# Kernel tuning notes

Hardware: AMD Instinct MI355X
Metric: run time of the kernel (lower is better)

Reference implementation:

```python
import jax, jax.numpy as jnp
import numpy as np

ROUTES = 1152
CAPS = 10
IN_CH = 8
OUT_CH = 16
BATCH = 256
NUM_ITER = 3


def setup_inputs() -> dict:
    key = jax.random.key(0)
    kx, kw = jax.random.split(key)
    x = jax.random.normal(kx, (BATCH, ROUTES, IN_CH), dtype=jnp.float32)
    # W corresponds to nn.Parameter of shape [1, routes, caps, out, in]; leading 1 dropped.
    W = jax.random.normal(kw, (ROUTES, CAPS, OUT_CH, IN_CH), dtype=jnp.float32)
    return {"x": x, "W": W}


def _squash(s):
    # Faithful to source: sum of squares over the trailing singleton dim -> elementwise.
    sq = s * s
    return sq * s / ((1.0 + sq) * jnp.sqrt(sq))


def reference(x, W):
    # u_hat[b,r,c,o] = W[r,c,o,i] @ x[b,r,i]
    u_hat = jnp.einsum("rcoi,bri->brco", W, x)
    b_ij = jnp.zeros((ROUTES, CAPS), dtype=x.dtype)
    v = None
    for it in range(NUM_ITER):
        # legacy F.softmax on 4D [1,R,C,1] tensor -> softmax over dim=1 (routes)
        c_ij = jax.nn.softmax(b_ij, axis=0)  # [R, C]
        s_j = jnp.einsum("rc,brco->bco", c_ij, u_hat)  # [B, C, O]
        v = _squash(s_j)
        if it < NUM_ITER - 1:
            # a_ij[b,r,c] = <u_hat[b,r,c,:], v[b,c,:]>; b_ij += mean over batch
            a_ij = jnp.einsum("brco,bco->brc", u_hat, v)
            b_ij = b_ij + a_ij.mean(axis=0)
    # original returns v_j.squeeze(1) with shape [B, caps, out, 1]
    return v[..., None]
```

## Files before the change

### kernel.cpp

```cpp
#include <hip/hip_runtime.h>
#include <math.h>

namespace {

constexpr int B_ = 256;
constexpr int R_ = 1152;
constexpr int C_ = 10;
constexpr int O_ = 16;
constexpr int I_ = 8;
constexpr int CO_ = C_ * O_;
constexpr int WRI_ = C_ * O_ * I_;

constexpr int KS2_ = 64;
constexpr int RC2_ = R_ / KS2_;
constexpr int RT_  = 4;
constexpr int NBLK_ = 640;

constexpr int KSF_ = 16;
constexpr int RCF_ = R_ / KSF_;
constexpr int MBF_ = 16;

constexpr size_t XT_OFF    = 0;
constexpr size_t XT_N      = (size_t)R_ * B_ * I_;
constexpr size_t SP_OFF    = XT_OFF + XT_N;
constexpr size_t SP_N      = (size_t)CO_ * KS2_ * B_;
constexpr size_t V_OFF     = SP_OFF + SP_N;
constexpr size_t V_N       = (size_t)B_ * CO_;
constexpr size_t BIJ_OFF   = V_OFF + V_N;
constexpr size_t BIJ_N     = (size_t)C_ * R_;
constexpr size_t FL_TOTAL  = BIJ_OFF + BIJ_N;

__device__ __forceinline__ float squashf(float s) {
    return s * fabsf(s) / (1.0f + s * s);
}

__global__ __launch_bounds__(256) void k_tr2(const float* __restrict__ x,
                                             float* __restrict__ xT,
                                             float* __restrict__ bijT) {
    __shared__ float t[8][32][8];
    const int tid = threadIdx.x;
    {
        const int gi = blockIdx.x * 256 + tid;
        if (gi < C_ * R_) bijT[gi] = 0.f;
    }
    const int r0 = (blockIdx.x % 36) * 32;
    const int b0 = (blockIdx.x / 36) * 8;
    {
        const int rl = tid & 31, bl = tid >> 5;
        const float4* p = (const float4*)(x + ((size_t)(b0 + bl) * R_ + (r0 + rl)) * I_);
        const float4 a0 = p[0], a1 = p[1];
        float* d = &t[bl][rl][0];
        *(float4*)d = a0;
        *(float4*)(d + 4) = a1;
    }
    __syncthreads();
    {
        const int f = tid & 7, rw = tid >> 3;
        const float* s8 = &t[f][rw][0];
        const float4 a0 = *(const float4*)s8, a1 = *(const float4*)(s8 + 4);
        float* d = xT + ((size_t)(r0 + rw) * B_ + (b0 + f)) * I_;
        *(float4*)d = a0;
        *(float4*)(d + 4) = a1;
    }
}

template <bool UNIFORM>
__global__ __launch_bounds__(256) void k_s5(const float* __restrict__ xT,
                                            const float* __restrict__ Wm,
                                            const float* __restrict__ bijT,
                                            float* __restrict__ spart) {
    __shared__ __align__(16) float wlds[RC2_ * 128];
    __shared__ float cwch[RC2_];
    __shared__ float sred[8];

    const int tid  = threadIdx.x;
    const int lane = tid & 63;
    const int c    = blockIdx.x;
    const int ks   = blockIdx.y;
    const int r0   = ks * RC2_;

    {
        const float4* src = (const float4*)(Wm + ((size_t)r0 * C_ + c) * 128);
        float4* dst = (float4*)wlds;
        #pragma unroll
        for (int k = 0; k < (RC2_ * 32 + 255) / 256; ++k) {
            const int idx = tid + 256 * k;
            if (idx < RC2_ * 32) {
                const int r = idx >> 5, q = idx & 31;
                dst[idx] = src[(size_t)r * (C_ * 32) + q];
            }
        }
    }

    if (!UNIFORM) {
        const float* bc = bijT + (size_t)c * R_;
        float bv[5];
        #pragma unroll
        for (int k = 0; k < 5; ++k) {
            const int r = tid + 256 * k;
            bv[k] = (r < R_) ? bc[r] : -1e30f;
        }
        float m = -1e30f;
        #pragma unroll
        for (int k = 0; k < 5; ++k) m = fmaxf(m, bv[k]);
        #pragma unroll
        for (int off = 32; off > 0; off >>= 1)
            m = fmaxf(m, __shfl_down(m, off, 64));
        if (lane == 0) sred[tid >> 6] = m;
        __syncthreads();
        const float bm = fmaxf(fmaxf(sred[0], sred[1]), fmaxf(sred[2], sred[3]));
        float se = 0.f;
        #pragma unroll
        for (int k = 0; k < 5; ++k)
            se += (bv[k] > -1e29f) ? expf(bv[k] - bm) : 0.f;
        #pragma unroll
        for (int off = 32; off > 0; off >>= 1)
            se += __shfl_down(se, off, 64);
        if (lane == 0) sred[4 + (tid >> 6)] = se;
        __syncthreads();
        const float inv = 1.0f / (sred[4] + sred[5] + sred[6] + sred[7]);
        if (tid < RC2_) cwch[tid] = expf(bc[r0 + tid] - bm) * inv;
    }
    __syncthreads();

    const int o0 = (tid >> 6) * 4;

    float acc[4][4];
    #pragma unroll
    for (int oo = 0; oo < 4; ++oo)
        #pragma unroll
        for (int bb = 0; bb < 4; ++bb) acc[oo][bb] = 0.f;

    const float* xbase = xT + ((size_t)r0 * B_ + lane) * I_;

    #pragma unroll 2
    for (int r = 0; r < RC2_; ++r) {
        const float cw = UNIFORM ? (1.0f / (float)R_) : cwch[r];
        float xs[4][8];
        #pragma unroll
        for (int bb = 0; bb < 4; ++bb) {
            const float4* xp =
                (const float4*)(xbase + (size_t)r * B_ * I_ + bb * 64 * I_);
            const float4 a0 = xp[0], a1 = xp[1];
            xs[bb][0] = a0.x * cw; xs[bb][1] = a0.y * cw;
            xs[bb][2] = a0.z * cw; xs[bb][3] = a0.w * cw;
            xs[bb][4] = a1.x * cw; xs[bb][5] = a1.y * cw;
            xs[bb][6] = a1.z * cw; xs[bb][7] = a1.w * cw;
        }
        const float4* wl = (const float4*)&wlds[r * 128 + o0 * 8];
        #pragma unroll
        for (int oo = 0; oo < 4; ++oo) {
            const float4 w0 = wl[oo * 2 + 0];
            const float4 w1 = wl[oo * 2 + 1];
            #pragma unroll
            for (int bb = 0; bb < 4; ++bb) {
                float a = acc[oo][bb];
                a = fmaf(xs[bb][0], w0.x, a);
                a = fmaf(xs[bb][1], w0.y, a);
                a = fmaf(xs[bb][2], w0.z, a);
                a = fmaf(xs[bb][3], w0.w, a);
                a = fmaf(xs[bb][4], w1.x, a);
                a = fmaf(xs[bb][5], w1.y, a);
                a = fmaf(xs[bb][6], w1.z, a);
                a = fmaf(xs[bb][7], w1.w, a);
                acc[oo][bb] = a;
            }
        }
    }

    float* sp = spart + (((size_t)(c * O_ + o0)) * KS2_ + ks) * B_ + lane;
    #pragma unroll
    for (int oo = 0; oo < 4; ++oo)
        #pragma unroll
        for (int bb = 0; bb < 4; ++bb)
            sp[(size_t)oo * KS2_ * B_ + bb * 64] = acc[oo][bb];
}

__global__ __launch_bounds__(256) void k_v3(const float* __restrict__ spart,
                                            float* __restrict__ vout) {
    __shared__ float sh[192];
    const int tid  = threadIdx.x;
    const int lane = tid & 63;
    const int g    = tid >> 6;
    const int co2  = blockIdx.x % CO_;
    const int bseg = blockIdx.x / CO_;
    const float* p = spart + (((size_t)co2) * KS2_ + g * 16) * B_ + bseg * 64 + lane;
    float t0 = 0.f, t1 = 0.f, t2 = 0.f, t3 = 0.f;
    #pragma unroll
    for (int j = 0; j < 16; j += 4) {
        t0 += p[(size_t)(j + 0) * B_];
        t1 += p[(size_t)(j + 1) * B_];
        t2 += p[(size_t)(j + 2) * B_];
        t3 += p[(size_t)(j + 3) * B_];
    }
    const float s = (t0 + t1) + (t2 + t3);
    if (g) sh[(g - 1) * 64 + lane] = s;
    __syncthreads();
    if (g == 0) {
        const float tot = s + sh[lane] + sh[64 + lane] + sh[128 + lane];
        const int b = bseg * 64 + lane;
        vout[(size_t)b * CO_ + co2] = squashf(tot);
    }
}

__global__ __launch_bounds__(640) void k_a4(const float* __restrict__ xT,
                                            const float* __restrict__ Wm,
                                            const float* __restrict__ v,
                                            float* __restrict__ bijT) {
    __shared__ __align__(16) float xrow[RT_ * B_ * I_];
    __shared__ float part[RT_][640];

    const int tid = threadIdx.x;
    const int r0  = blockIdx.x * RT_;

    for (int k = tid; k < RT_ * B_ * I_ / 4; k += 640)
        ((float4*)xrow)[k] = ((const float4*)(xT + (size_t)r0 * B_ * I_))[k];
    __syncthreads();

    const int co = tid % CO_;
    const int bg = tid / CO_;
    const int b0 = bg * 64;

    float acc[RT_][8];
    #pragma unroll
    for (int rr = 0; rr < RT_; ++rr)
        #pragma unroll
        for (int i = 0; i < 8; ++i) acc[rr][i] = 0.f;

    const float* vp = v + co;
    #pragma unroll 2
    for (int bb = 0; bb < 64; ++bb) {
        const int b = b0 + bb;
        const float vt = vp[(size_t)b * CO_];
        #pragma unroll
        for (int rr = 0; rr < RT_; ++rr) {
            const float4 y0 = *(const float4*)(&xrow[(rr * B_ + b) * I_]);
            const float4 y1 = *(const float4*)(&xrow[(rr * B_ + b) * I_ + 4]);
            acc[rr][0] = fmaf(vt, y0.x, acc[rr][0]);
            acc[rr][1] = fmaf(vt, y0.y, acc[rr][1]);
            acc[rr][2] = fmaf(vt, y0.z, acc[rr][2]);
            acc[rr][3] = fmaf(vt, y0.w, acc[rr][3]);
            acc[rr][4] = fmaf(vt, y1.x, acc[rr][4]);
            acc[rr][5] = fmaf(vt, y1.y, acc[rr][5]);
            acc[rr][6] = fmaf(vt, y1.z, acc[rr][6]);
            acc[rr][7] = fmaf(vt, y1.w, acc[rr][7]);
        }
    }

    #pragma unroll
    for (int rr = 0; rr < RT_; ++rr) {
        const float* wp = Wm + (((size_t)(r0 + rr)) * CO_ + co) * I_;
        const float4 w0 = *(const float4*)wp;
        const float4 w1 = *(const float4*)(wp + 4);
        const float p0 = fmaf(acc[rr][1], w0.y, acc[rr][0] * w0.x);
        const float p1 = fmaf(acc[rr][3], w0.w, acc[rr][2] * w0.z);
        const float p2 = fmaf(acc[rr][5], w1.y, acc[rr][4] * w1.x);
        const float p3 = fmaf(acc[rr][7], w1.w, acc[rr][6] * w1.z);
        part[rr][tid] = (p0 + p1) + (p2 + p3);
    }
    __syncthreads();

    if (tid < CO_) {
        #pragma unroll
        for (int rr = 0; rr < RT_; ++rr) {
            float a = part[rr][tid] + part[rr][CO_ + tid] +
                      part[rr][2 * CO_ + tid] + part[rr][3 * CO_ + tid];
            #pragma unroll
            for (int off = 8; off > 0; off >>= 1)
                a += __shfl_down(a, off, 16);
            if ((tid & 15) == 0)
                bijT[(size_t)(tid >> 4) * R_ + (r0 + rr)] += a * (1.0f / (float)B_);
        }
    }
}

template <bool UNIFORM>
__global__ __launch_bounds__(256) void k_s_f(const float* __restrict__ x,
                                             const float* __restrict__ Wm,
                                             const float* __restrict__ cij,
                                             float* __restrict__ s_out) {
    const int o  = threadIdx.x & 15;
    const int tb = threadIdx.x >> 4;
    const int b  = blockIdx.z * MBF_ + tb;
    const int c  = blockIdx.y;
    const int r0 = blockIdx.x * RCF_;

    const float* xp = x + ((size_t)b * R_ + r0) * I_;
    const float* wp = Wm + (((size_t)r0 * C_ + c) * O_ + o) * I_;
    const float* cp = cij + (size_t)r0 * C_ + c;

    float acc = 0.f;
    #pragma unroll 4
    for (int r = 0; r < RCF_; ++r) {
        const float4 xv0 = *(const float4*)(xp);
        const float4 xv1 = *(const float4*)(xp + 4);
        const float4 wv0 = *(const float4*)(wp);
        const float4 wv1 = *(const float4*)(wp + 4);
        const float p0 = fmaf(xv0.y, wv0.y, xv0.x * wv0.x);
        const float p1 = fmaf(xv0.w, wv0.w, xv0.z * wv0.z);
        const float p2 = fmaf(xv1.y, wv1.y, xv1.x * wv1.x);
        const float p3 = fmaf(xv1.w, wv1.w, xv1.z * wv1.z);
        const float cw = UNIFORM ? (1.0f / (float)R_) : cp[0];
        acc = fmaf(cw, (p0 + p1) + (p2 + p3), acc);
        xp += I_;
        wp += WRI_;
        cp += C_;
    }
    atomicAdd(&s_out[((size_t)b * C_ + c) * O_ + o], acc);
}

__global__ __launch_bounds__(256) void k_a_f(const float* __restrict__ x,
                                             const float* __restrict__ Wm,
                                             const float* __restrict__ s_in,
                                             float* __restrict__ amean) {
    __shared__ __align__(16) float wlds[2 * WRI_];
    __shared__ float red[4][2 * C_];

    const int tid = threadIdx.x;
    const int r0  = blockIdx.x * 2;

    const float* wsrc = Wm + (size_t)r0 * WRI_;
    #pragma unroll
    for (int k = 0; k < 2 * WRI_ / 256; ++k)
        wlds[tid + 256 * k] = wsrc[tid + 256 * k];
    __syncthreads();

    const int b    = tid;
    const int lane = tid & 63;
    const int wv   = tid >> 6;

    float xv[2][I_];
    const float4* xp4 = (const float4*)(x + ((size_t)b * R_ + r0) * I_);
    #pragma unroll
    for (int rr = 0; rr < 2; ++rr) {
        const float4 a0 = xp4[rr * 2 + 0];
        const float4 a1 = xp4[rr * 2 + 1];
        xv[rr][0] = a0.x; xv[rr][1] = a0.y; xv[rr][2] = a0.z; xv[rr][3] = a0.w;
        xv[rr][4] = a1.x; xv[rr][5] = a1.y; xv[rr][6] = a1.z; xv[rr][7] = a1.w;
    }

    #pragma unroll 1
    for (int c = 0; c < C_; ++c) {
        const float4* sp4 = (const float4*)(s_in + ((size_t)b * C_ + c) * O_);
        float v[O_];
        #pragma unroll
        for (int q = 0; q < 4; ++q) {
            const float4 sv = sp4[q];
            v[q * 4 + 0] = squashf(sv.x);
            v[q * 4 + 1] = squashf(sv.y);
            v[q * 4 + 2] = squashf(sv.z);
            v[q * 4 + 3] = squashf(sv.w);
        }
        #pragma unroll 1
        for (int rr = 0; rr < 2; ++rr) {
            const float4* wl4 = (const float4*)&wlds[(rr * C_ + c) * O_ * I_];
            float a = 0.f;
            #pragma unroll
            for (int o = 0; o < O_; ++o) {
                const float4 w0 = wl4[o * 2 + 0];
                const float4 w1 = wl4[o * 2 + 1];
                float u = xv[rr][0] * w0.x;
                u = fmaf(xv[rr][1], w0.y, u);
                u = fmaf(xv[rr][2], w0.z, u);
                u = fmaf(xv[rr][3], w0.w, u);
                u = fmaf(xv[rr][4], w1.x, u);
                u = fmaf(xv[rr][5], w1.y, u);
                u = fmaf(xv[rr][6], w1.z, u);
                u = fmaf(xv[rr][7], w1.w, u);
                a = fmaf(u, v[o], a);
            }
            #pragma unroll
            for (int off = 32; off > 0; off >>= 1)
                a += __shfl_down(a, off, 64);
            if (lane == 0) red[wv][rr * C_ + c] = a;
        }
    }

    __syncthreads();
    if (tid < 2 * C_) {
        const float t = red[0][tid] + red[1][tid] + red[2][tid] + red[3][tid];
        const int rr = tid / C_;
        const int c  = tid % C_;
        amean[(size_t)(r0 + rr) * C_ + c] = t * (1.0f / (float)B_);
    }
}

__global__ __launch_bounds__(256) void k_soft(const float* __restrict__ amean,
                                              float* __restrict__ bij,
                                              float* __restrict__ cij) {
    const int c   = blockIdx.x;
    const int tid = threadIdx.x;
    __shared__ float sred[4];

    float vals[5];
    float m = -1e30f;
    #pragma unroll
    for (int k = 0; k < 5; ++k) {
        const int r = tid + 256 * k;
        if (r < R_) {
            const size_t idx = (size_t)r * C_ + c;
            const float vv = bij[idx] + amean[idx];
            bij[idx] = vv;
            vals[k] = vv;
            m = fmaxf(m, vv);
        } else {
            vals[k] = -1e30f;
        }
    }
    #pragma unroll
    for (int off = 32; off > 0; off >>= 1)
        m = fmaxf(m, __shfl_down(m, off, 64));
    if ((tid & 63) == 0) sred[tid >> 6] = m;
    __syncthreads();
    const float bm = fmaxf(fmaxf(sred[0], sred[1]), fmaxf(sred[2], sred[3]));
    __syncthreads();

    float se = 0.f;
    #pragma unroll
    for (int k = 0; k < 5; ++k)
        se += (vals[k] > -1e29f) ? expf(vals[k] - bm) : 0.f;
    #pragma unroll
    for (int off = 32; off > 0; off >>= 1)
        se += __shfl_down(se, off, 64);
    if ((tid & 63) == 0) sred[tid >> 6] = se;
    __syncthreads();
    const float inv = 1.0f / (sred[0] + sred[1] + sred[2] + sred[3]);

    #pragma unroll
    for (int k = 0; k < 5; ++k) {
        const int r = tid + 256 * k;
        if (r < R_) cij[(size_t)r * C_ + c] = expf(vals[k] - bm) * inv;
    }
}

__global__ __launch_bounds__(256) void k_squash(float* __restrict__ s) {
    const int idx = blockIdx.x * 256 + threadIdx.x;
    if (idx < B_ * CO_) s[idx] = squashf(s[idx]);
}

}

extern "C" void kernel_launch(void* const* d_in, const int* in_sizes, int n_in,
                              void* d_out, int out_size, void* d_ws, size_t ws_size,
                              hipStream_t stream) {
    const float* x  = (const float*)d_in[0];
    const float* Wm = (const float*)d_in[1];
    float* out = (float*)d_out;
    float* ws  = (float*)d_ws;

    const size_t need = FL_TOTAL * sizeof(float);

    if (ws_size >= need) {
        float* xT    = ws + XT_OFF;
        float* spart = ws + SP_OFF;
        float* v     = ws + V_OFF;
        float* bijT  = ws + BIJ_OFF;

        const dim3 gs(C_, KS2_);

        k_tr2<<<1152, 256, 0, stream>>>(x, xT, bijT);

        k_s5<true><<<gs, 256, 0, stream>>>(xT, Wm, bijT, spart);
        k_v3<<<NBLK_, 256, 0, stream>>>(spart, v);
        k_a4<<<R_ / RT_, 640, 0, stream>>>(xT, Wm, v, bijT);

        k_s5<false><<<gs, 256, 0, stream>>>(xT, Wm, bijT, spart);
        k_v3<<<NBLK_, 256, 0, stream>>>(spart, v);
        k_a4<<<R_ / RT_, 640, 0, stream>>>(xT, Wm, v, bijT);

        k_s5<false><<<gs, 256, 0, stream>>>(xT, Wm, bijT, spart);
        k_v3<<<NBLK_, 256, 0, stream>>>(spart, out);
    } else {
        float* s_buf = ws;
        float* cij   = ws + 40960;
        float* bij   = cij + R_ * C_;
        float* amean = bij + R_ * C_;

        const dim3 gsf(KSF_, C_, B_ / MBF_);

        hipMemsetAsync(bij, 0, R_ * C_ * sizeof(float), stream);

        hipMemsetAsync(s_buf, 0, B_ * CO_ * sizeof(float), stream);
        k_s_f<true><<<gsf, 256, 0, stream>>>(x, Wm, cij, s_buf);
        k_a_f<<<R_ / 2, 256, 0, stream>>>(x, Wm, s_buf, amean);
        k_soft<<<C_, 256, 0, stream>>>(amean, bij, cij);

        hipMemsetAsync(s_buf, 0, B_ * CO_ * sizeof(float), stream);
        k_s_f<false><<<gsf, 256, 0, stream>>>(x, Wm, cij, s_buf);
        k_a_f<<<R_ / 2, 256, 0, stream>>>(x, Wm, s_buf, amean);
        k_soft<<<C_, 256, 0, stream>>>(amean, bij, cij);

        hipMemsetAsync(out, 0, B_ * CO_ * sizeof(float), stream);
        k_s_f<false><<<gsf, 256, 0, stream>>>(x, Wm, cij, out);
        k_squash<<<(B_ * CO_ + 255) / 256, 256, 0, stream>>>(out);
    }
}
```

Measured before the change: 208.0 us.

## Stage x tiles in swizzled LDS, split batch across blocks, fold softmax weights into W

The s-accumulation kernel now splits the batch into two halves via a third grid dimension and raises the route split from 64 to 72 chunks, giving many more blocks. Each block stages its x slice into LDS with an XOR swizzle to avoid bank conflicts, and folds the routing coefficient into W at load time instead of scaling x on every step. The reduction kernel is adjusted to sum 72 partials. Costs are a larger LDS footprint per block and more partial sums written and re-read.

```diff
diff --git a/kernel.cpp b/kernel.cpp
--- a/kernel.cpp
+++ b/kernel.cpp
@@ -11,8 +11,9 @@
 constexpr int CO_ = C_ * O_;
 constexpr int WRI_ = C_ * O_ * I_;
 
-constexpr int KS2_ = 64;
+constexpr int KS2_ = 72;
 constexpr int RC2_ = R_ / KS2_;
+constexpr int BH_  = 128;
 constexpr int RT_  = 4;
 constexpr int NBLK_ = 640;
 
@@ -69,7 +70,8 @@
                                             const float* __restrict__ Wm,
                                             const float* __restrict__ bijT,
                                             float* __restrict__ spart) {
-    __shared__ __align__(16) float wlds[RC2_ * 128];
+    __shared__ __align__(16) float4 xl[RC2_ * 256];
+    __shared__ __align__(16) float  wl[RC2_ * 128];
     __shared__ float cwch[RC2_];
     __shared__ float sred[8];
 
@@ -77,20 +79,8 @@
     const int lane = tid & 63;
     const int c    = blockIdx.x;
     const int ks   = blockIdx.y;
+    const int bh   = blockIdx.z;
     const int r0   = ks * RC2_;
-
-    {
-        const float4* src = (const float4*)(Wm + ((size_t)r0 * C_ + c) * 128);
-        float4* dst = (float4*)wlds;
-        #pragma unroll
-        for (int k = 0; k < (RC2_ * 32 + 255) / 256; ++k) {
-            const int idx = tid + 256 * k;
-            if (idx < RC2_ * 32) {
-                const int r = idx >> 5, q = idx & 31;
-                dst[idx] = src[(size_t)r * (C_ * 32) + q];
-            }
-        }
-    }
 
     if (!UNIFORM) {
         const float* bc = bijT + (size_t)c * R_;
@@ -123,56 +113,80 @@
     }
     __syncthreads();
 
+    {
+        const float4* src = (const float4*)(Wm + ((size_t)r0 * C_ + c) * 128);
+        float4* dst = (float4*)wl;
+        #pragma unroll
+        for (int k = 0; k < (RC2_ * 32) / 256; ++k) {
+            const int idx = tid + 256 * k;
+            const int r = idx >> 5, q = idx & 31;
+            float4 wv = src[(size_t)r * (C_ * 32) + q];
+            const float cw = UNIFORM ? (1.0f / (float)R_) : cwch[r];
+            wv.x *= cw; wv.y *= cw; wv.z *= cw; wv.w *= cw;
+            dst[idx] = wv;
+        }
+    }
+    {
+        const float4* src = (const float4*)(xT + ((size_t)r0 * B_ + bh * BH_) * I_);
+        #pragma unroll
+        for (int k = 0; k < (RC2_ * 256) / 256; ++k) {
+            const int idx = tid + 256 * k;
+            const int r = idx >> 8, er = idx & 255;
+            xl[r * 256 + (er ^ ((er >> 3) & 7))] = src[(size_t)r * 512 + er];
+        }
+    }
+    __syncthreads();
+
     const int o0 = (tid >> 6) * 4;
 
-    float acc[4][4];
+    const int e00 = (2 * lane) ^ ((lane >> 2) & 7);
+    const int e01 = e00 ^ 1;
+
+    float acc[4][2];
     #pragma unroll
     for (int oo = 0; oo < 4; ++oo)
         #pragma unroll
-        for (int bb = 0; bb < 4; ++bb) acc[oo][bb] = 0.f;
-
-    const float* xbase = xT + ((size_t)r0 * B_ + lane) * I_;
-
-    #pragma unroll 2
+        for (int bb = 0; bb < 2; ++bb) acc[oo][bb] = 0.f;
+
+    #pragma unroll 4
     for (int r = 0; r < RC2_; ++r) {
-        const float cw = UNIFORM ? (1.0f / (float)R_) : cwch[r];
-        float xs[4][8];
-        #pragma unroll
-        for (int bb = 0; bb < 4; ++bb) {
-            const float4* xp =
-                (const float4*)(xbase + (size_t)r * B_ * I_ + bb * 64 * I_);
-            const float4 a0 = xp[0], a1 = xp[1];
-            xs[bb][0] = a0.x * cw; xs[bb][1] = a0.y * cw;
-            xs[bb][2] = a0.z * cw; xs[bb][3] = a0.w * cw;
-            xs[bb][4] = a1.x * cw; xs[bb][5] = a1.y * cw;
-            xs[bb][6] = a1.z * cw; xs[bb][7] = a1.w * cw;
-        }
-        const float4* wl = (const float4*)&wlds[r * 128 + o0 * 8];
+        const int ra = r * 256;
+        const float4 a00 = xl[ra + e00];
+        const float4 a01 = xl[ra + e01];
+        const float4 a10 = xl[ra + 128 + e00];
+        const float4 a11 = xl[ra + 128 + e01];
+        float xr[2][8];
+        xr[0][0] = a00.x; xr[0][1] = a00.y; xr[0][2] = a00.z; xr[0][3] = a00.w;
+        xr[0][4] = a01.x; xr[0][5] = a01.y; xr[0][6] = a01.z; xr[0][7] = a01.w;
+        xr[1][0] = a10.x; xr[1][1] = a10.y; xr[1][2] = a10.z; xr[1][3] = a10.w;
+        xr[1][4] = a11.x; xr[1][5] = a11.y; xr[1][6] = a11.z; xr[1][7] = a11.w;
+
+        const float4* wp = (const float4*)&wl[r * 128 + o0 * 8];
         #pragma unroll
         for (int oo = 0; oo < 4; ++oo) {
-            const float4 w0 = wl[oo * 2 + 0];
-            const float4 w1 = wl[oo * 2 + 1];
+            const float4 w0 = wp[oo * 2 + 0];
+            const float4 w1 = wp[oo * 2 + 1];
             #pragma unroll
-            for (int bb = 0; bb < 4; ++bb) {
+            for (int bb = 0; bb < 2; ++bb) {
                 float a = acc[oo][bb];
-                a = fmaf(xs[bb][0], w0.x, a);
-                a = fmaf(xs[bb][1], w0.y, a);
-                a = fmaf(xs[bb][2], w0.z, a);
-                a = fmaf(xs[bb][3], w0.w, a);
-                a = fmaf(xs[bb][4], w1.x, a);
-                a = fmaf(xs[bb][5], w1.y, a);
-                a = fmaf(xs[bb][6], w1.z, a);
-                a = fmaf(xs[bb][7], w1.w, a);
+                a = fmaf(xr[bb][0], w0.x, a);
+                a = fmaf(xr[bb][1], w0.y, a);
+                a = fmaf(xr[bb][2], w0.z, a);
+                a = fmaf(xr[bb][3], w0.w, a);
+                a = fmaf(xr[bb][4], w1.x, a);
+                a = fmaf(xr[bb][5], w1.y, a);
+                a = fmaf(xr[bb][6], w1.z, a);
+                a = fmaf(xr[bb][7], w1.w, a);
                 acc[oo][bb] = a;
             }
         }
     }
 
-    float* sp = spart + (((size_t)(c * O_ + o0)) * KS2_ + ks) * B_ + lane;
+    float* sp = spart + (((size_t)(c * O_ + o0)) * KS2_ + ks) * B_ + bh * BH_ + lane;
     #pragma unroll
     for (int oo = 0; oo < 4; ++oo)
         #pragma unroll
-        for (int bb = 0; bb < 4; ++bb)
+        for (int bb = 0; bb < 2; ++bb)
             sp[(size_t)oo * KS2_ * B_ + bb * 64] = acc[oo][bb];
 }
 
@@ -184,16 +198,14 @@
     const int g    = tid >> 6;
     const int co2  = blockIdx.x % CO_;
     const int bseg = blockIdx.x / CO_;
-    const float* p = spart + (((size_t)co2) * KS2_ + g * 16) * B_ + bseg * 64 + lane;
-    float t0 = 0.f, t1 = 0.f, t2 = 0.f, t3 = 0.f;
-    #pragma unroll
-    for (int j = 0; j < 16; j += 4) {
+    const float* p = spart + (((size_t)co2) * KS2_ + g * 18) * B_ + bseg * 64 + lane;
+    float t0 = 0.f, t1 = 0.f;
+    #pragma unroll
+    for (int j = 0; j < 18; j += 2) {
         t0 += p[(size_t)(j + 0) * B_];
         t1 += p[(size_t)(j + 1) * B_];
-        t2 += p[(size_t)(j + 2) * B_];
-        t3 += p[(size_t)(j + 3) * B_];
-    }
-    const float s = (t0 + t1) + (t2 + t3);
+    }
+    const float s = t0 + t1;
     if (g) sh[(g - 1) * 64 + lane] = s;
     __syncthreads();
     if (g == 0) {
@@ -456,7 +468,7 @@
         float* v     = ws + V_OFF;
         float* bijT  = ws + BIJ_OFF;
 
-        const dim3 gs(C_, KS2_);
+        const dim3 gs(C_, KS2_, 2);
 
         k_tr2<<<1152, 256, 0, stream>>>(x, xT, bijT);
 
```

Measured after the change: 215.2 us. +3.5%, slower.
